# Performance work log

Hardware: AMD Instinct MI355X
Metric: run time of the kernel (lower is better)

## Reference

```python
import jax, jax.numpy as jnp
import numpy as np
from jax import lax

# ---- static config (matches init_kwargs) ----
STRIDE = 16
BASE_SIZE = 16
SCALES = np.array([2., 4., 8., 16., 32.])
RATIOS = np.array([0.5, 1., 2.])
CLIP = 4.14
NMS_THRESH = 0.7
PRE_NMS = 6000
POST_NMS = 300
MIN_SIZE = 16.0


def _whctrs(a):
    w = a[2] - a[0] + 1.0
    h = a[3] - a[1] + 1.0
    return w, h, a[0] + 0.5 * (w - 1.0), a[1] + 0.5 * (h - 1.0)


def _mkanchors(ws, hs, xc, yc):
    return np.stack([xc - 0.5 * (ws - 1.0), yc - 0.5 * (hs - 1.0),
                     xc + 0.5 * (ws - 1.0), yc + 0.5 * (hs - 1.0)], axis=1)


def _base_anchors():
    ba = np.array([1.0, 1.0, BASE_SIZE, BASE_SIZE]) - 1.0
    w, h, xc, yc = _whctrs(ba)
    size = w * h
    ws = np.round(np.sqrt(size / RATIOS))
    hs = np.round(ws * RATIOS)
    ra = _mkanchors(ws, hs, xc, yc)
    out = []
    for i in range(ra.shape[0]):
        w, h, xc, yc = _whctrs(ra[i])
        out.append(_mkanchors(w * SCALES, h * SCALES, xc, yc))
    return np.concatenate(out, axis=0)  # (A,4), A = len(ratios)*len(scales)


def _grid_anchors(Hf, Wf):
    ba = _base_anchors()                       # (A,4)
    sx, sy = np.meshgrid(np.arange(Wf) * STRIDE, np.arange(Hf) * STRIDE)
    shifts = np.stack([sx, sy, sx, sy], axis=-1)          # (Hf,Wf,4)
    anch = shifts[:, :, None, :] + ba[None, None, :, :]    # (Hf,Wf,A,4)
    return jnp.asarray(anch.reshape(1, -1, 4), dtype=jnp.float32)


def _decode_clip(anchors, deltas, img_h, img_w):
    # NormalizedBoxCenterDecoder (stds=1) + clip to image
    aw = anchors[..., 2] - anchors[..., 0]
    ah = anchors[..., 3] - anchors[..., 1]
    ax = anchors[..., 0] + 0.5 * aw
    ay = anchors[..., 1] + 0.5 * ah
    dx, dy, dw, dh = deltas[..., 0], deltas[..., 1], deltas[..., 2], deltas[..., 3]
    ox = dx * aw + ax
    oy = dy * ah + ay
    ow = jnp.exp(jnp.minimum(dw, CLIP)) * aw * 0.5
    oh = jnp.exp(jnp.minimum(dh, CLIP)) * ah * 0.5
    x1 = jnp.clip(ox - ow, 0.0, img_w - 1.0)
    y1 = jnp.clip(oy - oh, 0.0, img_h - 1.0)
    x2 = jnp.clip(ox + ow, 0.0, img_w - 1.0)
    y2 = jnp.clip(oy + oh, 0.0, img_h - 1.0)
    return jnp.stack([x1, y1, x2, y2], axis=-1)


def _nms_single(scores, boxes):
    # scores (N,), boxes (N,4). Greedy NMS, force_suppress, sorted by score desc.
    order = jnp.argsort(-scores)[:PRE_NMS]
    s = scores[order]
    b = boxes[order]
    x1, y1, x2, y2 = b[:, 0], b[:, 1], b[:, 2], b[:, 3]
    area = (x2 - x1) * (y2 - y1)
    iw = jnp.maximum(jnp.minimum(x2[:, None], x2[None, :]) - jnp.maximum(x1[:, None], x1[None, :]), 0.0)
    ih = jnp.maximum(jnp.minimum(y2[:, None], y2[None, :]) - jnp.maximum(y1[:, None], y1[None, :]), 0.0)
    inter = iw * ih
    iou = inter / (area[:, None] + area[None, :] - inter + 1e-12)  # (PRE,PRE)

    supp0 = s < 0.0  # invalid entries (score set to -1 by min_size filter)

    def body(supp, i):
        keep = jnp.logical_not(supp[i])
        new = jnp.where(keep, jnp.logical_or(supp, iou[i] > NMS_THRESH), supp)
        new = new.at[i].set(supp[i])  # never self-suppress
        return new, None

    supp, _ = lax.scan(body, supp0, jnp.arange(PRE_NMS))
    kept = jnp.logical_not(supp)
    perm = jnp.argsort(jnp.where(kept, 0, 1), stable=True)  # kept boxes first, order preserved
    out_s = jnp.where(kept[perm], s[perm], -1.0)
    out_b = jnp.where(kept[perm][:, None], b[perm], -1.0)
    return out_s[:POST_NMS, None], out_b[:POST_NMS]


def _forward(img, x, conv_w, conv_b, score_w, score_b, loc_w, loc_b):
    B, _, Hf, Wf = x.shape
    img_h, img_w = float(img.shape[2]), float(img.shape[3])
    anchors = _grid_anchors(Hf, Wf)  # (1, Hf*Wf*A, 4)

    # conv1 3x3 pad 1 + ReLU
    h = lax.conv_general_dilated(x, conv_w, (1, 1), [(1, 1), (1, 1)],
                                 dimension_numbers=('NCHW', 'OIHW', 'NCHW'))
    h = jax.nn.relu(h + conv_b[None, :, None, None])

    A = score_w.shape[0]
    raw_scores = jnp.einsum('bchw,oc->bhwo', h, score_w.reshape(A, -1)) + score_b
    raw_scores = raw_scores.reshape(B, -1, 1)                       # (B,N,1)
    raw_boxes = jnp.einsum('bchw,oc->bhwo', h, loc_w.reshape(4 * A, -1)) + loc_b
    raw_boxes = raw_boxes.reshape(B, -1, 4)                         # (B,N,4)

    rpn_scores = jax.nn.sigmoid(raw_scores)

    roi = _decode_clip(anchors, raw_boxes, img_h, img_w)            # (B,N,4)
    width = roi[..., 2] - roi[..., 0]
    height = roi[..., 3] - roi[..., 1]
    invalid = jnp.logical_or(width < MIN_SIZE, height < MIN_SIZE)   # (B,N)
    score = jnp.where(invalid[..., None], -1.0, rpn_scores)         # (B,N,1)
    roi = jnp.where(invalid[..., None], -1.0, roi)

    out_s, out_b = jax.vmap(_nms_single)(score[..., 0], roi)        # (B,300,1),(B,300,4)
    return jnp.concatenate([out_s, out_b], axis=-1)                 # (B,300,5)


def setup_inputs() -> dict:
    key = jax.random.key(0)
    ks = jax.random.split(key, 8)
    img = jax.random.normal(ks[0], (1, 3, 1024, 1024), jnp.float32)
    x = jax.random.normal(ks[1], (1, 1024, 64, 64), jnp.float32)
    conv_w = jax.random.normal(ks[2], (1024, 1024, 3, 3), jnp.float32) * 0.01
    conv_b = jnp.zeros((1024,), jnp.float32)
    score_w = jax.random.normal(ks[3], (15, 1024, 1, 1), jnp.float32) * 0.01
    score_b = jnp.zeros((15,), jnp.float32)
    loc_w = jax.random.normal(ks[4], (60, 1024, 1, 1), jnp.float32) * 0.002
    loc_b = jnp.zeros((60,), jnp.float32)
    return {"img": img, "x": x, "conv_w": conv_w, "conv_b": conv_b,
            "score_w": score_w, "score_b": score_b, "loc_w": loc_w, "loc_b": loc_b}


def reference(img, x, conv_w, conv_b, score_w, score_b, loc_w, loc_b):
    return _forward(img, x, conv_w, conv_b, score_w, score_b, loc_w, loc_b)
```

## Files before the change

kernel.cpp:

```cpp
#include <hip/hip_runtime.h>

typedef unsigned int uint;
typedef unsigned short ushort;
typedef unsigned long long u64;

typedef __attribute__((ext_vector_type(8))) short short8;
typedef __attribute__((ext_vector_type(4))) float floatx4;

__device__ inline ushort bf16rne(float v) {
  uint b = __float_as_uint(v);
  uint r = (b + 0x7fffu + ((b >> 16) & 1u)) >> 16;
  return (ushort)r;
}

__device__ inline void gl_lds16(const void* g, void* l) {
  __builtin_amdgcn_global_load_lds(
      (const __attribute__((address_space(1))) unsigned int*)g,
      (__attribute__((address_space(3))) unsigned int*)l, 16, 0, 0);
}

__global__ __launch_bounds__(256) void prep_x(const float* __restrict__ x,
                                              ushort* __restrict__ xh,
                                              ushort* __restrict__ xl) {
  __shared__ float tile[64 * 65];
  int ci0 = blockIdx.x * 64, y = blockIdx.y, t = threadIdx.x;
#pragma unroll
  for (int it = 0; it < 16; ++it) {
    int L = t + 256 * it;
    int cl = L >> 6, xx = L & 63;
    tile[cl * 65 + xx] = x[(size_t)(ci0 + cl) * 4096 + y * 64 + xx];
  }
  __syncthreads();
#pragma unroll
  for (int it = 0; it < 16; ++it) {
    int L = t + 256 * it;
    int xx = L >> 6, cl = L & 63;
    float v = tile[cl * 65 + xx];
    ushort h2 = bf16rne(v);
    float hf = __uint_as_float((uint)h2 << 16);
    ushort l2 = bf16rne(v - hf);
    size_t oi = ((size_t)((y + 1) * 66 + (xx + 1))) * 1024 + ci0 + cl;
    xh[oi] = h2;
    xl[oi] = l2;
  }
}

__global__ __launch_bounds__(256) void prep_w(const float* __restrict__ w,
                                              ushort* __restrict__ wh,
                                              ushort* __restrict__ wl) {
  __shared__ float tile[2304];
  int co = blockIdx.x, ci0 = blockIdx.y * 256, t = threadIdx.x;
  const float* src = w + ((size_t)co * 1024 + ci0) * 9;
  for (int i = t; i < 2304; i += 256) tile[i] = src[i];
  __syncthreads();
  int ci = ci0 + t;
#pragma unroll
  for (int off = 0; off < 9; ++off) {
    float v = tile[t * 9 + off];
    ushort h2 = bf16rne(v);
    float hf = __uint_as_float((uint)h2 << 16);
    ushort l2 = bf16rne(v - hf);
    size_t oi = ((size_t)off << 20) | ((size_t)co << 10) | (size_t)ci;
    wh[oi] = h2;
    wl[oi] = l2;
  }
}

__global__ __launch_bounds__(256) void prep_head(
    const float* __restrict__ score_w, const float* __restrict__ loc_w,
    const float* __restrict__ score_b, const float* __restrict__ loc_b,
    ushort* __restrict__ wh, ushort* __restrict__ wl, float* __restrict__ bh) {
  int idx = blockIdx.x * 256 + threadIdx.x;
  int o = idx >> 10, ci = idx & 1023;
  float v = 0.f;
  if (o < 15) v = score_w[o * 1024 + ci];
  else if (o < 75) v = loc_w[(o - 15) * 1024 + ci];
  ushort h2 = bf16rne(v);
  float hf = __uint_as_float((uint)h2 << 16);
  wh[idx] = h2;
  wl[idx] = bf16rne(v - hf);
  if (idx < 128) bh[idx] = (idx < 15) ? score_b[idx] : ((idx < 75) ? loc_b[idx - 15] : 0.f);
}

template <int IM2COL>
__global__ __launch_bounds__(256, 1) void gemm_bf16x3(
    const ushort* __restrict__ Ahi, const ushort* __restrict__ Alo,
    const ushort* __restrict__ Bhi, const ushort* __restrict__ Blo,
    const float* __restrict__ bias, int nChunks, float* __restrict__ outRaw,
    ushort* __restrict__ outHi, ushort* __restrict__ outLo) {
  __shared__ ushort sm[2 * 4 * 128 * 32];
  const int t = threadIdx.x;
  const int m0 = blockIdx.x * 128;
  const int n0 = blockIdx.y * 128;

  auto stage = [&](int kc, int bufIdx) {
    char* lds = (char*)sm + bufIdx * 32768;
    int off = 0, cc = 0, oy = 0, ox = 0;
    if (IM2COL) {
      off = kc >> 5;
      cc = (kc & 31) << 5;
      oy = off / 3;
      ox = off - 3 * oy;
    }
#pragma unroll
    for (int q = 0; q < 2; ++q) {
      int L = t + 256 * q, row = L >> 2, seg = L & 3;
      size_t aoff, boff;
      if (IM2COL) {
        int m = m0 + row, y = m >> 6, xq = m & 63;
        aoff = ((size_t)((y + oy) * 66 + (xq + ox)) * 1024 + (size_t)cc) * 2 + seg * 16;
        boff = (((size_t)off << 20) + ((size_t)(n0 + row) << 10) + (size_t)cc) * 2 + seg * 16;
      } else {
        aoff = (((size_t)(m0 + row) << 10) + (size_t)kc * 32) * 2 + seg * 16;
        boff = (((size_t)(n0 + row) << 10) + (size_t)kc * 32) * 2 + seg * 16;
      }
      int dst = L * 16;
      gl_lds16((const char*)Ahi + aoff, lds + dst);
      gl_lds16((const char*)Alo + aoff, lds + 8192 + dst);
      gl_lds16((const char*)Bhi + boff, lds + 16384 + dst);
      gl_lds16((const char*)Blo + boff, lds + 24576 + dst);
    }
  };

  const int lane = t & 63, wv = t >> 6;
  const int wm = (wv & 1) * 64, wn = (wv >> 1) * 64;
  const int arow = wm + (lane & 15);
  const int brow = wn + (lane & 15);
  const int ko = (lane >> 4) * 8;

  floatx4 acc[4][4];
#pragma unroll
  for (int i = 0; i < 4; ++i)
#pragma unroll
    for (int j = 0; j < 4; ++j) acc[i][j] = (floatx4){0.f, 0.f, 0.f, 0.f};

  stage(0, 0);
  for (int kc = 0; kc < nChunks; ++kc) {
    __syncthreads();
    if (kc + 1 < nChunks) stage(kc + 1, (kc + 1) & 1);
    const ushort* sb = sm + (kc & 1) * 16384;
    const ushort* sAh = sb;
    const ushort* sAl = sb + 4096;
    const ushort* sBh = sb + 8192;
    const ushort* sBl = sb + 12288;
    short8 ah[4], al[4], bh2[4], bl2[4];
#pragma unroll
    for (int i = 0; i < 4; ++i) {
      ah[i] = *(const short8*)(sAh + (arow + 16 * i) * 32 + ko);
      al[i] = *(const short8*)(sAl + (arow + 16 * i) * 32 + ko);
      bh2[i] = *(const short8*)(sBh + (brow + 16 * i) * 32 + ko);
      bl2[i] = *(const short8*)(sBl + (brow + 16 * i) * 32 + ko);
    }
#pragma unroll
    for (int i = 0; i < 4; ++i)
#pragma unroll
      for (int j = 0; j < 4; ++j) {
        acc[i][j] = __builtin_amdgcn_mfma_f32_16x16x32_bf16(ah[i], bh2[j], acc[i][j], 0, 0, 0);
        acc[i][j] = __builtin_amdgcn_mfma_f32_16x16x32_bf16(ah[i], bl2[j], acc[i][j], 0, 0, 0);
        acc[i][j] = __builtin_amdgcn_mfma_f32_16x16x32_bf16(al[i], bh2[j], acc[i][j], 0, 0, 0);
      }
  }

#pragma unroll
  for (int i = 0; i < 4; ++i)
#pragma unroll
    for (int j = 0; j < 4; ++j) {
      int nn = n0 + wn + 16 * j + (lane & 15);
      float bv = bias[nn];
#pragma unroll
      for (int r = 0; r < 4; ++r) {
        int mm = m0 + wm + 16 * i + (lane >> 4) * 4 + r;
        float v = acc[i][j][r] + bv;
        if (IM2COL) {
          v = fmaxf(v, 0.f);
          ushort h2 = bf16rne(v);
          float hf = __uint_as_float((uint)h2 << 16);
          ushort l2 = bf16rne(v - hf);
          outHi[(size_t)mm * 1024 + nn] = h2;
          outLo[(size_t)mm * 1024 + nn] = l2;
        } else {
          outRaw[(size_t)mm * 128 + nn] = v;
        }
      }
    }
}

__global__ __launch_bounds__(256) void decode_k(const float* __restrict__ raw,
                                                float* __restrict__ scores,
                                                float4* __restrict__ boxes,
                                                uint* __restrict__ key32,
                                                uint* __restrict__ hist) {
  int i = blockIdx.x * 256 + threadIdx.x;
  int m = i / 15, a = i - m * 15;
  int y = m >> 6, x = m & 63;
  const float* rp = raw + (size_t)m * 128;
  float logit = rp[a];
  float dx = rp[15 + 4 * a], dy = rp[16 + 4 * a];
  float dw = rp[17 + 4 * a], dh = rp[18 + 4 * a];
  int rr = a / 5, ss = a - rr * 5;
  float sc5 = (float)(2 << ss);
  float W = ((rr == 0) ? 23.f : (rr == 1) ? 16.f : 11.f) * sc5;
  float H = ((rr == 0) ? 12.f : (rr == 1) ? 16.f : 22.f) * sc5;
  float aw = W - 1.f, ah = H - 1.f;
  float ax = x * 16.f + 7.5f, ay = y * 16.f + 7.5f;
  float ox = dx * aw + ax, oyc = dy * ah + ay;
  float ow = expf(fminf(dw, 4.14f)) * aw * 0.5f;
  float oh = expf(fminf(dh, 4.14f)) * ah * 0.5f;
  float x1 = fminf(fmaxf(ox - ow, 0.f), 1023.f);
  float y1 = fminf(fmaxf(oyc - oh, 0.f), 1023.f);
  float x2 = fminf(fmaxf(ox + ow, 0.f), 1023.f);
  float y2 = fminf(fmaxf(oyc + oh, 0.f), 1023.f);
  bool inval = ((x2 - x1) < 16.f) || ((y2 - y1) < 16.f);
  float sc = inval ? -1.f : (1.f / (1.f + expf(-logit)));
  scores[i] = sc;
  boxes[i] = inval ? make_float4(-1.f, -1.f, -1.f, -1.f) : make_float4(x1, y1, x2, y2);
  uint kb = __float_as_uint(sc);
  uint key = (kb & 0x80000000u) ? ~kb : (kb | 0x80000000u);
  key32[i] = key;
  atomicAdd(&hist[key >> 16], 1u);
}

__global__ __launch_bounds__(1024) void scan_hist(const uint* __restrict__ hist,
                                                  uint* __restrict__ bbase,
                                                  uint* __restrict__ selC) {
  __shared__ uint cs[1024];
  int t = threadIdx.x;
  const uint* hp = hist + t * 64;
  uint s = 0;
#pragma unroll 8
  for (int i = 0; i < 64; ++i) s += hp[i];
  cs[t] = s;
  __syncthreads();
  for (int d = 1; d < 1024; d <<= 1) {
    uint v = cs[t] + ((t + d < 1024) ? cs[t + d] : 0u);
    __syncthreads();
    cs[t] = v;
    __syncthreads();
  }
  uint above = (t < 1023) ? cs[t + 1] : 0u;
  uint run = 0;
  for (int i = 63; i >= 0; --i) {
    uint h = hp[i];
    uint ca = above + run;
    bbase[t * 64 + i] = ca;
    if (ca < 6000u && ca + h >= 6000u) {
      selC[0] = (uint)(t * 64 + i);
      selC[1] = ca + h;
    }
    run += h;
  }
}

__global__ __launch_bounds__(256) void scatter_k(const uint* __restrict__ key32,
                                                 const uint* __restrict__ bbase,
                                                 const uint* __restrict__ selC,
                                                 uint* __restrict__ fill,
                                                 u64* __restrict__ sby) {
  int i = blockIdx.x * 256 + threadIdx.x;
  uint k = key32[i];
  uint b = k >> 16;
  if (b >= selC[0]) {
    uint pos = bbase[b] + atomicAdd(&fill[b], 1u);
    if (pos < 8192) sby[pos] = ((u64)k << 32) | (u64)(~(uint)i);
  }
}

__global__ __launch_bounds__(64) void bucket_sort(const uint* __restrict__ bbase,
                                                  const uint* __restrict__ selC,
                                                  u64* __restrict__ sby) {
  __shared__ u64 sk[4096];
  uint T = selC[0], C = selC[1];
  int lane = threadIdx.x;
  for (uint b = T + blockIdx.x; b < 65536u; b += 8192u) {
    uint base = bbase[b];
    if (base >= 6000u) continue;
    uint incl = (b == 0) ? C : bbase[b - 1];
    uint n = incl - base;
    if (n < 2u || n > 4096u) continue;
    if (base + n > 8192u) continue;
    uint np2 = 1;
    while (np2 < n) np2 <<= 1;
    for (uint j = lane; j < np2; j += 64) sk[j] = (j < n) ? sby[base + j] : 0ull;
    __syncthreads();
    for (uint k = 2; k <= np2; k <<= 1) {
      for (uint j2 = k >> 1; j2 > 0; j2 >>= 1) {
        for (uint p = lane; p < (np2 >> 1); p += 64) {
          uint i1 = ((p & ~(j2 - 1)) << 1) | (p & (j2 - 1));
          uint ix = i1 | j2;
          u64 a = sk[i1], c = sk[ix];
          bool descseg = (i1 & k) == 0;
          if ((a < c) == descseg) { sk[i1] = c; sk[ix] = a; }
        }
        __syncthreads();
      }
    }
    for (uint j = lane; j < n; j += 64) sby[base + j] = sk[j];
    __syncthreads();
  }
}

__global__ __launch_bounds__(256) void gather_sorted(
    const u64* __restrict__ sby, const float* __restrict__ scores,
    const float4* __restrict__ boxes, float* __restrict__ sortedS,
    float4* __restrict__ sortedB) {
  int j = blockIdx.x * 256 + threadIdx.x;
  if (j >= 6016) return;
  if (j < 6000) {
    u64 key = sby[j];
    uint idx = ~(uint)(key & 0xffffffffu);
    if (idx >= 61440u) idx = 61439u;
    sortedS[j] = scores[idx];
    sortedB[j] = boxes[idx];
  } else {
    sortedS[j] = -1.f;
    sortedB[j] = make_float4(0.f, 0.f, 0.f, 0.f);
  }
}

__global__ __launch_bounds__(64) void iou_mask(const float4* __restrict__ boxes,
                                               u64* __restrict__ mask) {
  __shared__ float cx1[64], cy1[64], cx2[64], cy2[64], car[64];
  int bi = blockIdx.x, bj = blockIdx.y, t = threadIdx.x;
  float4 cb = boxes[bj * 64 + t];
  cx1[t] = cb.x; cy1[t] = cb.y; cx2[t] = cb.z; cy2[t] = cb.w;
  car[t] = (cb.z - cb.x) * (cb.w - cb.y);
  __syncthreads();
  int r = bi * 64 + t;
  float4 rb = boxes[r];
  float ra = (rb.z - rb.x) * (rb.w - rb.y);
  u64 wd = 0;
#pragma unroll 8
  for (int j = 0; j < 64; ++j) {
    float iw = fmaxf(fminf(rb.z, cx2[j]) - fmaxf(rb.x, cx1[j]), 0.f);
    float ih = fmaxf(fminf(rb.w, cy2[j]) - fmaxf(rb.y, cy1[j]), 0.f);
    float inter = iw * ih;
    float iou = inter / (ra + car[j] - inter + 1e-12f);
    if (iou > 0.7f && r != bj * 64 + j) wd |= (1ull << j);
  }
  mask[(size_t)r * 128 + bj] = wd;
}

__global__ __launch_bounds__(64) void nms_scan(const u64* __restrict__ mask,
                                               const float* __restrict__ sortedS,
                                               const float4* __restrict__ sortedB,
                                               float* __restrict__ out) {
  __shared__ int klist[304];
  int lane = threadIdx.x;
  u64 Sx = 0, Sy = 0;
  for (int w2 = 0; w2 < 94; ++w2) {
    bool neg = sortedS[w2 * 64 + lane] < 0.f;
    u64 m2 = __ballot(neg);
    if ((w2 >> 1) == lane) { if (w2 & 1) Sy = m2; else Sx = m2; }
  }
  int count = 0;
  for (int w2 = 0; w2 < 94 && count < 300; ++w2) {
    u64 cur = __shfl((w2 & 1) ? Sy : Sx, w2 >> 1);
    u64 rem = ~cur;
    if (w2 == 93) rem &= (1ull << 48) - 1;
    int pf_i = -1;
    ulonglong2 pf;
    while (rem) {
      int b = __builtin_ctzll(rem);
      int i = w2 * 64 + b;
      u64 rem2 = (b == 63) ? 0ull : (rem & (~0ull << (b + 1)));
      ulonglong2 rv;
      if (i == pf_i) rv = pf;
      else rv = ((const ulonglong2*)(mask + (size_t)i * 128))[lane];
      if (rem2) {
        int nb = __builtin_ctzll(rem2);
        pf_i = w2 * 64 + nb;
        pf = ((const ulonglong2*)(mask + (size_t)pf_i * 128))[lane];
      } else {
        pf_i = -1;
      }
      if (lane == 0) klist[count] = i;
      count++;
      if (count == 300) break;
      Sx |= rv.x;
      Sy |= rv.y;
      u64 cur2 = __shfl((w2 & 1) ? Sy : Sx, w2 >> 1);
      rem = rem2 & ~cur2;
    }
  }
  __syncthreads();
  for (int j = lane; j < 300; j += 64) {
    float s;
    float4 bb;
    if (j < count) {
      int i = klist[j];
      s = sortedS[i];
      bb = sortedB[i];
    } else {
      s = -1.f;
      bb = make_float4(-1.f, -1.f, -1.f, -1.f);
    }
    out[j * 5 + 0] = s;
    out[j * 5 + 1] = bb.x;
    out[j * 5 + 2] = bb.y;
    out[j * 5 + 3] = bb.z;
    out[j * 5 + 4] = bb.w;
  }
}

constexpr size_t O_XH = 0;
constexpr size_t O_XL = 8921088;
constexpr size_t O_WTH = 17842176;
constexpr size_t O_WTL = 36716544;
constexpr size_t O_HH = 55590912;
constexpr size_t O_HL = 63979520;
constexpr size_t O_WHH = 72368128;
constexpr size_t O_WHL = 72630272;
constexpr size_t O_BHD = 72892416;
constexpr size_t O_SC = 72892928;
constexpr size_t O_BX = 73138688;
constexpr size_t O_KEY = 74121728;
constexpr size_t O_HIST = 74367488;
constexpr size_t O_BBASE = 74629632;
constexpr size_t O_SELC = 74891776;
constexpr size_t O_SBY = 74892032;
constexpr size_t O_SS = 74957568;
constexpr size_t O_SB = 74981632;
constexpr size_t O_RAW = 0;
constexpr size_t O_MASK = 17842176;

extern "C" void kernel_launch(void* const* d_in, const int* in_sizes, int n_in,
                              void* d_out, int out_size, void* d_ws,
                              size_t ws_size, hipStream_t stream) {
  (void)in_sizes; (void)n_in; (void)out_size; (void)ws_size;
  const float* x = (const float*)d_in[1];
  const float* conv_w = (const float*)d_in[2];
  const float* conv_b = (const float*)d_in[3];
  const float* score_w = (const float*)d_in[4];
  const float* score_b = (const float*)d_in[5];
  const float* loc_w = (const float*)d_in[6];
  const float* loc_b = (const float*)d_in[7];
  float* out = (float*)d_out;
  char* ws = (char*)d_ws;

  ushort* xh = (ushort*)(ws + O_XH);
  ushort* xl = (ushort*)(ws + O_XL);
  ushort* wTh = (ushort*)(ws + O_WTH);
  ushort* wTl = (ushort*)(ws + O_WTL);
  ushort* hh = (ushort*)(ws + O_HH);
  ushort* hl = (ushort*)(ws + O_HL);
  ushort* wHh = (ushort*)(ws + O_WHH);
  ushort* wHl = (ushort*)(ws + O_WHL);
  float* biasH = (float*)(ws + O_BHD);
  float* raw = (float*)(ws + O_RAW);
  float* scores = (float*)(ws + O_SC);
  float4* boxes = (float4*)(ws + O_BX);
  uint* key32 = (uint*)(ws + O_KEY);
  uint* hist = (uint*)(ws + O_HIST);
  uint* bbase = (uint*)(ws + O_BBASE);
  uint* selC = (uint*)(ws + O_SELC);
  u64* sby = (u64*)(ws + O_SBY);
  float* sortedS = (float*)(ws + O_SS);
  float4* sortedB = (float4*)(ws + O_SB);
  u64* mask = (u64*)(ws + O_MASK);

  hipMemsetAsync(ws + O_XH, 0, 2 * 8921088, stream);
  hipMemsetAsync(ws + O_HIST, 0, 262144, stream);

  prep_x<<<dim3(16, 64), 256, 0, stream>>>(x, xh, xl);
  prep_w<<<dim3(1024, 4), 256, 0, stream>>>(conv_w, wTh, wTl);
  prep_head<<<512, 256, 0, stream>>>(score_w, loc_w, score_b, loc_b, wHh, wHl, biasH);

  gemm_bf16x3<1><<<dim3(32, 8), 256, 0, stream>>>(xh, xl, wTh, wTl, conv_b, 288,
                                                  nullptr, hh, hl);
  gemm_bf16x3<0><<<dim3(32, 1), 256, 0, stream>>>(hh, hl, wHh, wHl, biasH, 32,
                                                  raw, nullptr, nullptr);

  decode_k<<<240, 256, 0, stream>>>(raw, scores, boxes, key32, hist);
  scan_hist<<<1, 1024, 0, stream>>>(hist, bbase, selC);
  hipMemsetAsync(ws + O_HIST, 0, 262144, stream);
  scatter_k<<<240, 256, 0, stream>>>(key32, bbase, selC, hist, sby);
  bucket_sort<<<8192, 64, 0, stream>>>(bbase, selC, sby);
  gather_sorted<<<24, 256, 0, stream>>>(sby, scores, boxes, sortedS, sortedB);
  iou_mask<<<dim3(94, 94), 64, 0, stream>>>(sortedB, mask);
  nms_scan<<<1, 64, 0, stream>>>(mask, sortedS, sortedB, out);
}
```

Baseline: 820.4 us.

## Shrink GEMM N-tile, swizzle LDS layout, rank-sort buckets, skip lower IoU tiles

The conv GEMM tile drops from 128x128 to 128x64 and the launch bound rises to two blocks per CU, so the 256-block grid becomes 512 blocks with better CU coverage. The LDS staging is laid out per 16-row fragment, so each lane reads its fragment contiguously. The bitonic bucket sort, which ran as 8192 mostly idle blocks, is replaced by a 256-block rank sort that counts larger keys for each element. iou_mask now skips tiles below the diagonal, since greedy NMS only needs suppression of later boxes. The costs are lower reuse per tile and a quadratic rank pass on large buckets, and rank sort needs unique keys, which the stored index provides.

Result: slower. 1.051 ms (+28.1%).

```diff
diff --git a/kernel.cpp b/kernel.cpp
--- a/kernel.cpp
+++ b/kernel.cpp
@@ -83,18 +83,18 @@
 }
 
 template <int IM2COL>
-__global__ __launch_bounds__(256, 1) void gemm_bf16x3(
+__global__ __launch_bounds__(256, 2) void gemm_bf16x3(
     const ushort* __restrict__ Ahi, const ushort* __restrict__ Alo,
     const ushort* __restrict__ Bhi, const ushort* __restrict__ Blo,
     const float* __restrict__ bias, int nChunks, float* __restrict__ outRaw,
     ushort* __restrict__ outHi, ushort* __restrict__ outLo) {
-  __shared__ ushort sm[2 * 4 * 128 * 32];
+  __shared__ ushort sm[2 * 12288];
   const int t = threadIdx.x;
   const int m0 = blockIdx.x * 128;
-  const int n0 = blockIdx.y * 128;
+  const int n0 = blockIdx.y * 64;
 
   auto stage = [&](int kc, int bufIdx) {
-    char* lds = (char*)sm + bufIdx * 32768;
+    char* lds = (char*)sm + bufIdx * 24576;
     int off = 0, cc = 0, oy = 0, ox = 0;
     if (IM2COL) {
       off = kc >> 5;
@@ -104,57 +104,69 @@
     }
 #pragma unroll
     for (int q = 0; q < 2; ++q) {
-      int L = t + 256 * q, row = L >> 2, seg = L & 3;
-      size_t aoff, boff;
+      int L = t + 256 * q;
+      int g = L >> 6, ko = (L >> 4) & 3, row = L & 15;
+      int gr = g * 16 + row;
+      size_t aoff;
       if (IM2COL) {
-        int m = m0 + row, y = m >> 6, xq = m & 63;
-        aoff = ((size_t)((y + oy) * 66 + (xq + ox)) * 1024 + (size_t)cc) * 2 + seg * 16;
-        boff = (((size_t)off << 20) + ((size_t)(n0 + row) << 10) + (size_t)cc) * 2 + seg * 16;
+        int m = m0 + gr, y = m >> 6, xq = m & 63;
+        aoff = ((size_t)((y + oy) * 66 + (xq + ox)) * 1024 + (size_t)cc + ko * 8) * 2;
       } else {
-        aoff = (((size_t)(m0 + row) << 10) + (size_t)kc * 32) * 2 + seg * 16;
-        boff = (((size_t)(n0 + row) << 10) + (size_t)kc * 32) * 2 + seg * 16;
+        aoff = (((size_t)(m0 + gr) << 10) + (size_t)kc * 32 + ko * 8) * 2;
       }
-      int dst = L * 16;
-      gl_lds16((const char*)Ahi + aoff, lds + dst);
-      gl_lds16((const char*)Alo + aoff, lds + 8192 + dst);
-      gl_lds16((const char*)Bhi + boff, lds + 16384 + dst);
-      gl_lds16((const char*)Blo + boff, lds + 24576 + dst);
+      gl_lds16((const char*)Ahi + aoff, lds + L * 16);
+      gl_lds16((const char*)Alo + aoff, lds + 8192 + L * 16);
+    }
+    {
+      int L = t;
+      int g = L >> 6, ko = (L >> 4) & 3, row = L & 15;
+      int gr = g * 16 + row;
+      size_t boff;
+      if (IM2COL) {
+        boff = (((size_t)off << 20) + ((size_t)(n0 + gr) << 10) + (size_t)cc + ko * 8) * 2;
+      } else {
+        boff = (((size_t)(n0 + gr) << 10) + (size_t)kc * 32 + ko * 8) * 2;
+      }
+      gl_lds16((const char*)Bhi + boff, lds + 16384 + L * 16);
+      gl_lds16((const char*)Blo + boff, lds + 20480 + L * 16);
     }
   };
 
   const int lane = t & 63, wv = t >> 6;
-  const int wm = (wv & 1) * 64, wn = (wv >> 1) * 64;
-  const int arow = wm + (lane & 15);
-  const int brow = wn + (lane & 15);
-  const int ko = (lane >> 4) * 8;
-
-  floatx4 acc[4][4];
+  const int wm = (wv & 1) * 64, wn = (wv >> 1) * 32;
+
+  floatx4 acc[4][2];
 #pragma unroll
   for (int i = 0; i < 4; ++i)
 #pragma unroll
-    for (int j = 0; j < 4; ++j) acc[i][j] = (floatx4){0.f, 0.f, 0.f, 0.f};
+    for (int j = 0; j < 2; ++j) acc[i][j] = (floatx4){0.f, 0.f, 0.f, 0.f};
 
   stage(0, 0);
   for (int kc = 0; kc < nChunks; ++kc) {
     __syncthreads();
     if (kc + 1 < nChunks) stage(kc + 1, (kc + 1) & 1);
-    const ushort* sb = sm + (kc & 1) * 16384;
+    const ushort* sb = sm + (kc & 1) * 12288;
     const ushort* sAh = sb;
     const ushort* sAl = sb + 4096;
     const ushort* sBh = sb + 8192;
-    const ushort* sBl = sb + 12288;
-    short8 ah[4], al[4], bh2[4], bl2[4];
+    const ushort* sBl = sb + 10240;
+    short8 ah[4], al[4], bh2[2], bl2[2];
 #pragma unroll
     for (int i = 0; i < 4; ++i) {
-      ah[i] = *(const short8*)(sAh + (arow + 16 * i) * 32 + ko);
-      al[i] = *(const short8*)(sAl + (arow + 16 * i) * 32 + ko);
-      bh2[i] = *(const short8*)(sBh + (brow + 16 * i) * 32 + ko);
-      bl2[i] = *(const short8*)(sBl + (brow + 16 * i) * 32 + ko);
+      int ga = (wm >> 4) + i;
+      ah[i] = *(const short8*)(sAh + ga * 512 + lane * 8);
+      al[i] = *(const short8*)(sAl + ga * 512 + lane * 8);
+    }
+#pragma unroll
+    for (int j = 0; j < 2; ++j) {
+      int gb = (wn >> 4) + j;
+      bh2[j] = *(const short8*)(sBh + gb * 512 + lane * 8);
+      bl2[j] = *(const short8*)(sBl + gb * 512 + lane * 8);
     }
 #pragma unroll
     for (int i = 0; i < 4; ++i)
 #pragma unroll
-      for (int j = 0; j < 4; ++j) {
+      for (int j = 0; j < 2; ++j) {
         acc[i][j] = __builtin_amdgcn_mfma_f32_16x16x32_bf16(ah[i], bh2[j], acc[i][j], 0, 0, 0);
         acc[i][j] = __builtin_amdgcn_mfma_f32_16x16x32_bf16(ah[i], bl2[j], acc[i][j], 0, 0, 0);
         acc[i][j] = __builtin_amdgcn_mfma_f32_16x16x32_bf16(al[i], bh2[j], acc[i][j], 0, 0, 0);
@@ -164,7 +176,7 @@
 #pragma unroll
   for (int i = 0; i < 4; ++i)
 #pragma unroll
-    for (int j = 0; j < 4; ++j) {
+    for (int j = 0; j < 2; ++j) {
       int nn = n0 + wn + 16 * j + (lane & 15);
       float bv = bias[nn];
 #pragma unroll
@@ -265,37 +277,28 @@
   }
 }
 
-__global__ __launch_bounds__(64) void bucket_sort(const uint* __restrict__ bbase,
-                                                  const uint* __restrict__ selC,
-                                                  u64* __restrict__ sby) {
+__global__ __launch_bounds__(256) void bucket_rank(const uint* __restrict__ bbase,
+                                                   const uint* __restrict__ selC,
+                                                   u64* __restrict__ sby) {
   __shared__ u64 sk[4096];
   uint T = selC[0], C = selC[1];
-  int lane = threadIdx.x;
-  for (uint b = T + blockIdx.x; b < 65536u; b += 8192u) {
+  int t = threadIdx.x;
+  for (uint b = T + blockIdx.x; b < 65536u; b += 256u) {
     uint base = bbase[b];
     if (base >= 6000u) continue;
     uint incl = (b == 0) ? C : bbase[b - 1];
     uint n = incl - base;
     if (n < 2u || n > 4096u) continue;
     if (base + n > 8192u) continue;
-    uint np2 = 1;
-    while (np2 < n) np2 <<= 1;
-    for (uint j = lane; j < np2; j += 64) sk[j] = (j < n) ? sby[base + j] : 0ull;
     __syncthreads();
-    for (uint k = 2; k <= np2; k <<= 1) {
-      for (uint j2 = k >> 1; j2 > 0; j2 >>= 1) {
-        for (uint p = lane; p < (np2 >> 1); p += 64) {
-          uint i1 = ((p & ~(j2 - 1)) << 1) | (p & (j2 - 1));
-          uint ix = i1 | j2;
-          u64 a = sk[i1], c = sk[ix];
-          bool descseg = (i1 & k) == 0;
-          if ((a < c) == descseg) { sk[i1] = c; sk[ix] = a; }
-        }
-        __syncthreads();
-      }
-    }
-    for (uint j = lane; j < n; j += 64) sby[base + j] = sk[j];
+    for (uint j = t; j < n; j += 256) sk[j] = sby[base + j];
     __syncthreads();
+    for (uint e = t; e < n; e += 256) {
+      u64 K = sk[e];
+      uint rank = 0;
+      for (uint j = 0; j < n; ++j) rank += (sk[j] > K) ? 1u : 0u;
+      sby[base + rank] = K;
+    }
   }
 }
 
@@ -319,8 +322,10 @@
 
 __global__ __launch_bounds__(64) void iou_mask(const float4* __restrict__ boxes,
                                                u64* __restrict__ mask) {
+  int bi = blockIdx.x, bj = blockIdx.y;
+  if (bj < bi) return;
   __shared__ float cx1[64], cy1[64], cx2[64], cy2[64], car[64];
-  int bi = blockIdx.x, bj = blockIdx.y, t = threadIdx.x;
+  int t = threadIdx.x;
   float4 cb = boxes[bj * 64 + t];
   cx1[t] = cb.x; cy1[t] = cb.y; cx2[t] = cb.z; cy2[t] = cb.w;
   car[t] = (cb.z - cb.x) * (cb.w - cb.y);
@@ -465,16 +470,16 @@
   prep_w<<<dim3(1024, 4), 256, 0, stream>>>(conv_w, wTh, wTl);
   prep_head<<<512, 256, 0, stream>>>(score_w, loc_w, score_b, loc_b, wHh, wHl, biasH);
 
-  gemm_bf16x3<1><<<dim3(32, 8), 256, 0, stream>>>(xh, xl, wTh, wTl, conv_b, 288,
-                                                  nullptr, hh, hl);
-  gemm_bf16x3<0><<<dim3(32, 1), 256, 0, stream>>>(hh, hl, wHh, wHl, biasH, 32,
+  gemm_bf16x3<1><<<dim3(32, 16), 256, 0, stream>>>(xh, xl, wTh, wTl, conv_b,
+                                                   288, nullptr, hh, hl);
+  gemm_bf16x3<0><<<dim3(32, 2), 256, 0, stream>>>(hh, hl, wHh, wHl, biasH, 32,
                                                   raw, nullptr, nullptr);
 
   decode_k<<<240, 256, 0, stream>>>(raw, scores, boxes, key32, hist);
   scan_hist<<<1, 1024, 0, stream>>>(hist, bbase, selC);
   hipMemsetAsync(ws + O_HIST, 0, 262144, stream);
   scatter_k<<<240, 256, 0, stream>>>(key32, bbase, selC, hist, sby);
-  bucket_sort<<<8192, 64, 0, stream>>>(bbase, selC, sby);
+  bucket_rank<<<256, 256, 0, stream>>>(bbase, selC, sby);
   gather_sorted<<<24, 256, 0, stream>>>(sby, scores, boxes, sortedS, sortedB);
   iou_mask<<<dim3(94, 94), 64, 0, stream>>>(sortedB, mask);
   nms_scan<<<1, 64, 0, stream>>>(mask, sortedS, sortedB, out);
```
